# Performance work log

Measured on AMD Instinct MI355X. Metric: run time of the kernel, lower is better.

## Reference

```python
import jax, jax.numpy as jnp
import numpy as np

NP, LP, ROUTINGS = 8, 16, 3
PAD = 2  # (kernel_size - 1) // 2 for kernel_size=5, stride=1


def _squash_2(t):
    # norm over LP axis (axis=3); torch: norm/(1+norm^2+1e-4) * t
    norm = jnp.linalg.norm(t, axis=3, keepdims=True)
    return norm / (1.0 + norm * norm + 1e-4) * t


def setup_inputs() -> dict:
    key = jax.random.key(0)
    k1, k2 = jax.random.split(key)
    x = jax.random.normal(k1, (4, 4, 16, 256, 256), dtype=jnp.float32)
    # conv weights initialized uniform [0, 0.1] as in the torch module
    W = jax.random.uniform(k2, (NP * LP, 16, 5, 5), dtype=jnp.float32) * 0.1
    return {"x": x, "W": W}


def reference(x, W):
    B, NC, LC, H, Wd = x.shape
    xf = x.reshape(B * NC, LC, H, Wd)
    votes = jax.lax.conv_general_dilated(
        xf, W, window_strides=(1, 1), padding=((PAD, PAD), (PAD, PAD)),
        dimension_numbers=("NCHW", "OIHW", "NCHW"))  # (B*NC, NP*LP, H, W)
    votes = votes.reshape(B, NC, NP, LP, H, Wd)
    sims = jnp.zeros((B, NC, NP, 1, H, Wd), dtype=x.dtype)
    parent = None
    for _ in range(ROUTINGS):
        c_ij = jax.nn.softmax(sims + 1e-4, axis=2)          # softmax over NP
        parent_bs = jnp.sum(c_ij * votes, axis=1, keepdims=True)  # sum over NC
        parent = _squash_2(parent_bs)                        # (B,1,NP,LP,H,W)
        sims = sims + jnp.sum(votes * parent, axis=3, keepdims=True)
    return parent[:, 0]  # squeeze NC axis -> (B, NP, LP, H, W)
```

## Files before the change

kernel.cpp:

```cpp
#include <hip/hip_runtime.h>

#define NPAR 8
#define LPAR 16
#define OCH 128
#define HH 256
#define WW 256
#define HWSZ (HH*WW)

typedef _Float16 f16x8 __attribute__((ext_vector_type(8)));
typedef _Float16 f16x4 __attribute__((ext_vector_type(4)));
typedef _Float16 f16x2 __attribute__((ext_vector_type(2)));
typedef float    f32x4 __attribute__((ext_vector_type(4)));

#define SMEM_MAIN 16896
#define VROW 132
#define SMEM_HALVES_FUSED 16896

#if defined(__has_builtin)
#if __has_builtin(__builtin_amdgcn_fdot2)
#define HAVE_FDOT2 1
#endif
#if __has_builtin(__builtin_amdgcn_global_load_lds)
#define HAVE_GLL 1
#endif
#endif

__device__ __forceinline__ float fdot2_acc(f16x2 a, f16x2 b, float c) {
#ifdef HAVE_FDOT2
    return __builtin_amdgcn_fdot2(a, b, c, false);
#else
    return c + (float)a[0] * (float)b[0] + (float)a[1] * (float)b[1];
#endif
}

__device__ __forceinline__ f16x2 quad_sum4_pk(f16x2 v) {
    int t = __builtin_amdgcn_update_dpp(0, __builtin_bit_cast(int, v),
                                        0xB1, 0xF, 0xF, true);
    v = v + __builtin_bit_cast(f16x2, t);
    t = __builtin_amdgcn_update_dpp(0, __builtin_bit_cast(int, v),
                                    0x4E, 0xF, 0xF, true);
    v = v + __builtin_bit_cast(f16x2, t);
    return v;
}

__device__ __forceinline__ void stage16(const _Float16* gp, _Float16* lp, int lane) {
#ifdef HAVE_GLL
    __builtin_amdgcn_global_load_lds((const __attribute__((address_space(1))) void*)gp,
                                     (__attribute__((address_space(3))) void*)lp, 16, 0, 0);
#else
    *(f16x8*)(lp + lane * 8) = *(const f16x8*)gp;
#endif
}

__global__ void reorder_W_lin(const float* __restrict__ Wg,
                              _Float16* __restrict__ ws) {
    int idx = blockIdx.x * 256 + threadIdx.x;
    if (idx >= 13 * 128 * 32) return;
    const int q  = idx & 31;
    const int oc = (idx >> 5) & 127;
    const int kk = idx >> 12;
    const int tap = 2 * kk + (q >> 4);
    const int ci  = ((q >> 3) & 1) * 8 + (q & 7);
    const float v = (tap < 25) ? Wg[oc * 400 + ci * 25 + tap] : 0.f;
    ws[idx] = (_Float16)v;
}

__global__ __launch_bounds__(256)
void transpose_x_kernel(const float* __restrict__ x, _Float16* __restrict__ xh) {
    __shared__ _Float16 ts[4096];
    const int tid = threadIdx.x;
    const int bx  = blockIdx.x;
    const int b   = bx >> 10;
    const int h   = (bx >> 2) & 255;
    const int wt  = bx & 3;
    const int w0  = wt * 64;
    {
        const int wl = tid & 63, cq = tid >> 6;
        const float* src = x + (((size_t)(b * 64 + cq * 16) * 256 + h) * 256 + w0 + wl);
#pragma unroll
        for (int k = 0; k < 2; ++k) {
            f16x8 pk;
#pragma unroll
            for (int j = 0; j < 8; ++j)
                pk[j] = (_Float16)src[(size_t)(k * 8 + j) * HWSZ];
            const int gL = (cq * 2 + k) ^ (wl & 7);
            *(f16x8*)&ts[wl * 64 + gL * 8] = pk;
        }
    }
    __syncthreads();
    {
        const int wo = tid >> 2, gq = tid & 3;
        _Float16* dst = xh + (((size_t)(b * 260) + h + 2) * 260 + (w0 + wo + 2)) * 64 + gq * 16;
#pragma unroll
        for (int k = 0; k < 2; ++k) {
            const int gL = (gq * 2 + k) ^ (wo & 7);
            *(f16x8*)&dst[k * 8] = *(const f16x8*)&ts[wo * 64 + gL * 8];
        }
    }
}

__global__ __launch_bounds__(256, 3)
void capsule_mfma10_kernel(const _Float16* __restrict__ xh,
                           const _Float16* __restrict__ wsW,
                           float* __restrict__ out) {
    __shared__ _Float16 sm[SMEM_MAIN];

    const int tid = threadIdx.x;
    const int w   = tid >> 6;
    const int l   = tid & 63;

    const int blk   = ((blockIdx.x & 7) << 10) + (blockIdx.x >> 3);
    const int b     = blk >> 11;
    const int rt    = blk & 2047;
    const int hrow0 = (rt >> 4) << 1;
    const int w0    = (rt & 15) << 4;

    {
        const size_t bbase = ((size_t)(b * 260 + hrow0) * 260 + w0) * 64;
#pragma unroll
        for (int jj = 0; jj < 4; ++jj) {
            const int cidx = w * 4 + jj;
            if (cidx < 15) {
                const int G = cidx * 64 + l;
                const unsigned dyr = (unsigned)G / 160u;
                const unsigned rem = (unsigned)G - dyr * 160u;
                const int wp = rem >> 3, g = rem & 7;
                const int gsrc = g ^ (wp & 7);
                const _Float16* gp = xh + bbase + dyr * 16640u + wp * 64 + gsrc * 8;
                stage16(gp, &sm[cidx * 512], l);
            }
        }
    }
    __syncthreads();

    const int rwc = w >> 1;
    const int oh  = w & 1;
    const int kq  = l >> 4;
    const int ml  = l & 15;
    const bool hiT = (kq & 2) != 0;
    const int pxA = ml >> 2;
    const int colA = (ml & 3) * 16 + (kq & 1) * 8;
    const int bfbase = (oh * 64 + ml) * 32 + kq * 8;

    f32x4 acc[4][4];
#pragma unroll
    for (int a = 0; a < 4; ++a)
#pragma unroll
        for (int bb = 0; bb < 4; ++bb)
            acc[a][bb] = (f32x4){0.f, 0.f, 0.f, 0.f};

#pragma unroll
    for (int kk = 0; kk < 13; ++kk) {
        f16x8 bf[4];
#pragma unroll
        for (int bb = 0; bb < 4; ++bb)
            bf[bb] = *(const f16x8*)&wsW[kk * 4096 + bb * 512 + bfbase];

        const int t0 = 2 * kk;
        const int t1 = (2 * kk + 1 > 24) ? 24 : 2 * kk + 1;
        const int dy = hiT ? (t1 / 5) : (t0 / 5);
        const int dx = hiT ? (t1 % 5) : (t0 % 5);

        f16x8 af[4];
#pragma unroll
        for (int a = 0; a < 4; ++a) {
            const int wp = a * 4 + pxA + dx;
            af[a] = *(const f16x8*)&sm[((rwc + dy) * 20 + wp) * 64
                                       + (colA ^ ((wp & 7) << 3))];
        }
        __builtin_amdgcn_s_setprio(1);
#pragma unroll
        for (int a = 0; a < 4; ++a)
#pragma unroll
            for (int bb = 0; bb < 4; ++bb)
                acc[a][bb] = __builtin_amdgcn_mfma_f32_16x16x32_f16(
                    af[a], bf[bb], acc[a][bb], 0, 0, 0);
        __builtin_amdgcn_s_setprio(0);
    }
    __syncthreads();

#pragma unroll
    for (int a = 0; a < 4; ++a) {
#pragma unroll
        for (int reg = 0; reg < 4; ++reg) {
            f16x4 pk;
#pragma unroll
            for (int bb = 0; bb < 4; ++bb) pk[bb] = (_Float16)acc[a][bb][reg];
            const int R = rwc * 64 + a * 16 + kq * 4 + reg;
            *(f16x4*)&sm[R * VROW + ml * 8 + oh * 4] = pk;
        }
    }
    __syncthreads();

    const int ncR = tid & 3;
    const int h   = (tid >> 2) & 1;
    const int pxx = (tid >> 3) & 15;
    const int rw  = tid >> 7;

    const int R = rw * 64 + pxx * 4 + ncR;
    f16x8 vh[8];
#pragma unroll
    for (int c8 = 0; c8 < 8; ++c8)
        vh[c8] = *(const f16x8*)&sm[R * VROW + (h * 8 + c8) * 8];

    float* outb = out + (size_t)b * OCH * HWSZ
                + (size_t)(hrow0 + rw) * WW + (w0 + pxx);

    float sims[NPAR];
#pragma unroll
    for (int i = 0; i < NPAR; ++i) sims[i] = 0.f;

#pragma unroll
    for (int it = 0; it < 3; ++it) {
        float e[NPAR];
        float inv = 0.f;
        if (it > 0) {
            float mx = fmaxf(fmaxf(fmaxf(sims[0], sims[1]), fmaxf(sims[2], sims[3])),
                             fmaxf(fmaxf(sims[4], sims[5]), fmaxf(sims[6], sims[7])));
            float se = 0.f;
#pragma unroll
            for (int i = 0; i < NPAR; ++i) { e[i] = __expf(sims[i] - mx); se += e[i]; }
            inv = 1.f / se;
        }
#pragma unroll
        for (int np_ = 0; np_ < NPAR; ++np_) {
            const float cf = (it == 0) ? 0.f : e[np_] * inv;
            const f16x2 cp = (f16x2){(_Float16)cf, (_Float16)cf};
            float n2 = 0.f, dot = 0.f;
            f16x2 keep0 = (f16x2){(_Float16)0.f, (_Float16)0.f};
            f16x2 keep1 = keep0;
#pragma unroll
            for (int k = 0; k < 4; ++k) {
                const f16x2 vv = (f16x2){vh[2 * k][np_], vh[2 * k + 1][np_]};
                const f16x2 sv = (it == 0) ? vv : (cp * vv);
                const f16x2 t2 = quad_sum4_pk(sv);
                n2 = fdot2_acc(t2, t2, n2);
                if (it < 2) dot = fdot2_acc(vv, t2, dot);
                if (it == 2 && (k >> 1) == (ncR & 1)) {
                    if (k & 1) keep1 = t2; else keep0 = t2;
                }
            }
            n2 += __shfl_xor(n2, 4);
            if (it == 0) n2 *= 0.015625f;
            const float scale = sqrtf(n2) / (1.f + n2 + 1e-4f);
            if (it < 2) {
                dot += __shfl_xor(dot, 4);
                if (it == 0) dot *= 0.125f;
                sims[np_] += scale * dot;
            }
            if (it == 2 && (ncR >> 1) == h) {
                outb[(size_t)(np_ * LPAR + ncR * 4 + 0) * HWSZ] = scale * (float)keep0[0];
                outb[(size_t)(np_ * LPAR + ncR * 4 + 1) * HWSZ] = scale * (float)keep0[1];
                outb[(size_t)(np_ * LPAR + ncR * 4 + 2) * HWSZ] = scale * (float)keep1[0];
                outb[(size_t)(np_ * LPAR + ncR * 4 + 3) * HWSZ] = scale * (float)keep1[1];
            }
        }
    }
}

__device__ __forceinline__ int xs_addr6(int dyr, int wp, int col) {
    return (dyr * 20 + wp) * 64 + (col ^ ((wp & 7) << 3));
}

__global__ __launch_bounds__(256, 3)
void capsule_mfma6_kernel(const float* __restrict__ x,
                          const _Float16* __restrict__ wsf,
                          float* __restrict__ out) {
    __shared__ _Float16 sm[SMEM_HALVES_FUSED];

    const int tid = threadIdx.x;
    const int w   = tid >> 6;
    const int l   = tid & 63;

    const int blk   = ((blockIdx.x & 7) << 10) + (blockIdx.x >> 3);
    const int b     = blk >> 11;
    const int rt    = blk & 2047;
    const int hrow0 = (rt >> 4) << 1;
    const int w0    = (rt & 15) << 4;

    for (int i = 0; i < 15; ++i) {
        const unsigned idx = i * 256 + tid;
        const unsigned q   = idx / 20u;
        const int wp  = idx - q * 20u;
        const int cip = q & 7;
        const int t2  = q >> 3;
        const int nc  = t2 & 3;
        const int dyr = t2 >> 2;
        const int hh  = hrow0 + dyr - 2;
        const int wg  = w0 + wp - 2;
        const bool ok = (hh >= 0) && (hh < HH) && (wg >= 0) && (wg < WW);
        const float* src = x + (((size_t)(b * 4 + nc) * 16 + cip * 2) * HH + hh) * (size_t)WW + wg;
        const float v0 = ok ? src[0] : 0.f;
        const float v1 = ok ? src[HWSZ] : 0.f;
        *(f16x2*)&sm[xs_addr6(dyr, wp, nc * 16 + cip * 2)] =
            (f16x2){(_Float16)v0, (_Float16)v1};
    }
    __syncthreads();

    const int rwc = w >> 1;
    const int oh  = w & 1;
    const int p   = l >> 4;
    const int ml  = l & 15;
    const bool hiT = (p & 2) != 0;
    const int ciA = (p & 1) * 8;
    const int pxA = ml >> 2;
    const int ncA = ml & 3;
    const int bfbase = (oh * 64 + ml) * 32 + p * 8;

    f32x4 acc[4][4];
#pragma unroll
    for (int a = 0; a < 4; ++a)
#pragma unroll
        for (int bb = 0; bb < 4; ++bb)
            acc[a][bb] = (f32x4){0.f, 0.f, 0.f, 0.f};

#pragma unroll
    for (int kk = 0; kk < 13; ++kk) {
        f16x8 bf[4];
#pragma unroll
        for (int bb = 0; bb < 4; ++bb)
            bf[bb] = *(const f16x8*)&wsf[kk * 4096 + bb * 512 + bfbase];

        const int t0 = 2 * kk;
        const int t1 = (2 * kk + 1 > 24) ? 24 : 2 * kk + 1;
        const int dy = hiT ? (t1 / 5) : (t0 / 5);
        const int dx = hiT ? (t1 % 5) : (t0 % 5);

        f16x8 af[4];
#pragma unroll
        for (int a = 0; a < 4; ++a)
            af[a] = *(const f16x8*)&sm[xs_addr6(rwc + dy, a * 4 + pxA + dx, ncA * 16 + ciA)];

#pragma unroll
        for (int a = 0; a < 4; ++a)
#pragma unroll
            for (int bb = 0; bb < 4; ++bb)
                acc[a][bb] = __builtin_amdgcn_mfma_f32_16x16x32_f16(
                    af[a], bf[bb], acc[a][bb], 0, 0, 0);
    }
    __syncthreads();

#pragma unroll
    for (int a = 0; a < 4; ++a) {
#pragma unroll
        for (int reg = 0; reg < 4; ++reg) {
            f16x4 pk;
#pragma unroll
            for (int bb = 0; bb < 4; ++bb) pk[bb] = (_Float16)acc[a][bb][reg];
            const int R = rwc * 64 + a * 16 + p * 4 + reg;
            *(f16x4*)&sm[R * VROW + ml * 8 + oh * 4] = pk;
        }
    }
    __syncthreads();

    const int ncR = tid & 3;
    const int h   = (tid >> 2) & 1;
    const int pxx = (tid >> 3) & 15;
    const int rw  = tid >> 7;

    const int R = rw * 64 + pxx * 4 + ncR;
    f16x8 vh[8];
#pragma unroll
    for (int c8 = 0; c8 < 8; ++c8)
        vh[c8] = *(const f16x8*)&sm[R * VROW + (h * 8 + c8) * 8];

    float* outb = out + (size_t)b * OCH * HWSZ
                + (size_t)(hrow0 + rw) * WW + (w0 + pxx);

    float sims[NPAR];
#pragma unroll
    for (int i = 0; i < NPAR; ++i) sims[i] = 0.f;

#pragma unroll
    for (int it = 0; it < 3; ++it) {
        float mx = fmaxf(fmaxf(fmaxf(sims[0], sims[1]), fmaxf(sims[2], sims[3])),
                         fmaxf(fmaxf(sims[4], sims[5]), fmaxf(sims[6], sims[7])));
        float e[NPAR];
        float se = 0.f;
#pragma unroll
        for (int i = 0; i < NPAR; ++i) { e[i] = __expf(sims[i] - mx); se += e[i]; }
        const float inv = 1.f / se;

#pragma unroll
        for (int np_ = 0; np_ < NPAR; ++np_) {
            const float cf = e[np_] * inv;
            const f16x2 cp = (f16x2){(_Float16)cf, (_Float16)cf};
            float n2 = 0.f, dot = 0.f;
            f16x2 keep0 = (f16x2){(_Float16)0.f, (_Float16)0.f};
            f16x2 keep1 = keep0;
#pragma unroll
            for (int k = 0; k < 4; ++k) {
                const f16x2 vv = (f16x2){vh[2 * k][np_], vh[2 * k + 1][np_]};
                const f16x2 t2 = quad_sum4_pk(cp * vv);
                n2  = fdot2_acc(t2, t2, n2);
                dot = fdot2_acc(vv, t2, dot);
                if (it == 2 && (k >> 1) == (ncR & 1)) {
                    if (k & 1) keep1 = t2; else keep0 = t2;
                }
            }
            n2  += __shfl_xor(n2, 4);
            dot += __shfl_xor(dot, 4);
            const float scale = sqrtf(n2) / (1.f + n2 + 1e-4f);
            sims[np_] += scale * dot;

            if (it == 2 && (ncR >> 1) == h) {
                outb[(size_t)(np_ * LPAR + ncR * 4 + 0) * HWSZ] = scale * (float)keep0[0];
                outb[(size_t)(np_ * LPAR + ncR * 4 + 1) * HWSZ] = scale * (float)keep0[1];
                outb[(size_t)(np_ * LPAR + ncR * 4 + 2) * HWSZ] = scale * (float)keep1[0];
                outb[(size_t)(np_ * LPAR + ncR * 4 + 3) * HWSZ] = scale * (float)keep1[1];
            }
        }
    }
}

extern "C" void kernel_launch(void* const* d_in, const int* in_sizes, int n_in,
                              void* d_out, int out_size, void* d_ws, size_t ws_size,
                              hipStream_t stream) {
    const float* x  = (const float*)d_in[0];
    const float* Wg = (const float*)d_in[1];
    float* out = (float*)d_out;
    _Float16* ws = (_Float16*)d_ws;
    (void)in_sizes; (void)n_in; (void)out_size;

    const size_t XH_BYTES = (size_t)4 * 260 * 260 * 64 * 2;
    const size_t NEED = 131072 + XH_BYTES;

    hipLaunchKernelGGL(reorder_W_lin, dim3(208), dim3(256), 0, stream, Wg, ws);

    if (ws_size >= NEED) {
        _Float16* xh = ws + 65536;
        hipMemsetAsync((void*)xh, 0, XH_BYTES, stream);
        hipLaunchKernelGGL(transpose_x_kernel, dim3(4096), dim3(256), 0, stream, x, xh);
        hipLaunchKernelGGL(capsule_mfma10_kernel, dim3(8192), dim3(256), 0, stream,
                           xh, ws, out);
    } else {
        hipLaunchKernelGGL(capsule_mfma6_kernel, dim3(8192), dim3(256), 0, stream,
                           x, ws, out);
    }
}
```

Measured before the change: 219.2 us.

## Switch conv to 32x32x16 MFMA reading activations directly from global

Replaces the 16x16x32 MFMA tiling over paired taps with 32x32x16 MFMAs, one per tap over 16 channels, using a new per-tap weight layout (reorder_W25). The LDS staging of the input tile and its barrier are removed, and A fragments are loaded straight from the padded fp16 global buffer, relying on L1/L2 caching. The channel-to-parent mapping changes, so a perm-based repack of votes and a remapped output index are added. It drops the zero-padded 26th tap and an LDS round trip, at the cost of more global load traffic and less explicit reuse.

```diff
diff --git a/kernel.cpp b/kernel.cpp
--- a/kernel.cpp
+++ b/kernel.cpp
@@ -11,6 +11,8 @@
 typedef _Float16 f16x4 __attribute__((ext_vector_type(4)));
 typedef _Float16 f16x2 __attribute__((ext_vector_type(2)));
 typedef float    f32x4 __attribute__((ext_vector_type(4)));
+typedef float    f32x16 __attribute__((ext_vector_type(16)));
+typedef int      i32x4 __attribute__((ext_vector_type(4)));
 
 #define SMEM_MAIN 16896
 #define VROW 132
@@ -20,8 +22,8 @@
 #if __has_builtin(__builtin_amdgcn_fdot2)
 #define HAVE_FDOT2 1
 #endif
-#if __has_builtin(__builtin_amdgcn_global_load_lds)
-#define HAVE_GLL 1
+#if __has_builtin(__builtin_amdgcn_perm)
+#define HAVE_PERM 1
 #endif
 #endif
 
@@ -43,13 +45,14 @@
     return v;
 }
 
-__device__ __forceinline__ void stage16(const _Float16* gp, _Float16* lp, int lane) {
-#ifdef HAVE_GLL
-    __builtin_amdgcn_global_load_lds((const __attribute__((address_space(1))) void*)gp,
-                                     (__attribute__((address_space(3))) void*)lp, 16, 0, 0);
-#else
-    *(f16x8*)(lp + lane * 8) = *(const f16x8*)gp;
-#endif
+__global__ void reorder_W25(const float* __restrict__ Wg,
+                            _Float16* __restrict__ ws) {
+    int idx = blockIdx.x * 256 + threadIdx.x;
+    if (idx >= 25 * 128 * 16) return;
+    const int ci  = idx & 15;
+    const int oc  = (idx >> 4) & 127;
+    const int tap = idx >> 11;
+    ws[idx] = (_Float16)Wg[oc * 400 + ci * 25 + tap];
 }
 
 __global__ void reorder_W_lin(const float* __restrict__ Wg,
@@ -100,8 +103,8 @@
 }
 
 __global__ __launch_bounds__(256, 3)
-void capsule_mfma10_kernel(const _Float16* __restrict__ xh,
-                           const _Float16* __restrict__ wsW,
+void capsule_mfma11_kernel(const _Float16* __restrict__ xh,
+                           const _Float16* __restrict__ wsB,
                            float* __restrict__ out) {
     __shared__ _Float16 sm[SMEM_MAIN];
 
@@ -115,79 +118,52 @@
     const int hrow0 = (rt >> 4) << 1;
     const int w0    = (rt & 15) << 4;
 
-    {
-        const size_t bbase = ((size_t)(b * 260 + hrow0) * 260 + w0) * 64;
-#pragma unroll
-        for (int jj = 0; jj < 4; ++jj) {
-            const int cidx = w * 4 + jj;
-            if (cidx < 15) {
-                const int G = cidx * 64 + l;
-                const unsigned dyr = (unsigned)G / 160u;
-                const unsigned rem = (unsigned)G - dyr * 160u;
-                const int wp = rem >> 3, g = rem & 7;
-                const int gsrc = g ^ (wp & 7);
-                const _Float16* gp = xh + bbase + dyr * 16640u + wp * 64 + gsrc * 8;
-                stage16(gp, &sm[cidx * 512], l);
-            }
-        }
-    }
-    __syncthreads();
-
     const int rwc = w >> 1;
     const int oh  = w & 1;
-    const int kq  = l >> 4;
-    const int ml  = l & 15;
-    const bool hiT = (kq & 2) != 0;
-    const int pxA = ml >> 2;
-    const int colA = (ml & 3) * 16 + (kq & 1) * 8;
-    const int bfbase = (oh * 64 + ml) * 32 + kq * 8;
-
-    f32x4 acc[4][4];
-#pragma unroll
-    for (int a = 0; a < 4; ++a)
-#pragma unroll
-        for (int bb = 0; bb < 4; ++bb)
-            acc[a][bb] = (f32x4){0.f, 0.f, 0.f, 0.f};
-
-#pragma unroll
-    for (int kk = 0; kk < 13; ++kk) {
-        f16x8 bf[4];
-#pragma unroll
-        for (int bb = 0; bb < 4; ++bb)
-            bf[bb] = *(const f16x8*)&wsW[kk * 4096 + bb * 512 + bfbase];
-
-        const int t0 = 2 * kk;
-        const int t1 = (2 * kk + 1 > 24) ? 24 : 2 * kk + 1;
-        const int dy = hiT ? (t1 / 5) : (t0 / 5);
-        const int dx = hiT ? (t1 % 5) : (t0 % 5);
-
-        f16x8 af[4];
-#pragma unroll
-        for (int a = 0; a < 4; ++a) {
-            const int wp = a * 4 + pxA + dx;
-            af[a] = *(const f16x8*)&sm[((rwc + dy) * 20 + wp) * 64
-                                       + (colA ^ ((wp & 7) << 3))];
-        }
+    const int l31 = l & 31;
+    const int kh  = l >> 5;
+    const int ncA = l31 & 3;
+    const int pxq = l31 >> 2;
+
+    const _Float16* gb = xh + (((size_t)(b * 260 + hrow0 + rwc)) * 260 + w0 + pxq) * 64
+                       + ncA * 16 + kh * 8;
+    const _Float16* bP[5] = { gb, gb + 16640, gb + 2 * 16640, gb + 3 * 16640, gb + 4 * 16640 };
+
+    const _Float16* wbase = wsB + (oh * 64 + l31) * 16 + kh * 8;
+
+    f32x16 acc[2][2];
+#pragma unroll
+    for (int mt = 0; mt < 2; ++mt)
+#pragma unroll
+        for (int nt = 0; nt < 2; ++nt)
+#pragma unroll
+            for (int r = 0; r < 16; ++r)
+                acc[mt][nt][r] = 0.f;
+
+#pragma unroll
+    for (int tap = 0; tap < 25; ++tap) {
+        const int dy = tap / 5;
+        const int dx = tap % 5;
+        const f16x8 bf0 = *(const f16x8*)(wbase + tap * 2048);
+        const f16x8 bf1 = *(const f16x8*)(wbase + tap * 2048 + 512);
+        const f16x8 af0 = *(const f16x8*)(bP[dy] + (size_t)(dx)      * 64);
+        const f16x8 af1 = *(const f16x8*)(bP[dy] + (size_t)(dx + 8)  * 64);
         __builtin_amdgcn_s_setprio(1);
-#pragma unroll
-        for (int a = 0; a < 4; ++a)
-#pragma unroll
-            for (int bb = 0; bb < 4; ++bb)
-                acc[a][bb] = __builtin_amdgcn_mfma_f32_16x16x32_f16(
-                    af[a], bf[bb], acc[a][bb], 0, 0, 0);
+        acc[0][0] = __builtin_amdgcn_mfma_f32_32x32x16_f16(af0, bf0, acc[0][0], 0, 0, 0);
+        acc[0][1] = __builtin_amdgcn_mfma_f32_32x32x16_f16(af0, bf1, acc[0][1], 0, 0, 0);
+        acc[1][0] = __builtin_amdgcn_mfma_f32_32x32x16_f16(af1, bf0, acc[1][0], 0, 0, 0);
+        acc[1][1] = __builtin_amdgcn_mfma_f32_32x32x16_f16(af1, bf1, acc[1][1], 0, 0, 0);
         __builtin_amdgcn_s_setprio(0);
     }
-    __syncthreads();
-
-#pragma unroll
-    for (int a = 0; a < 4; ++a) {
-#pragma unroll
-        for (int reg = 0; reg < 4; ++reg) {
-            f16x4 pk;
-#pragma unroll
-            for (int bb = 0; bb < 4; ++bb) pk[bb] = (_Float16)acc[a][bb][reg];
-            const int R = rwc * 64 + a * 16 + kq * 4 + reg;
-            *(f16x4*)&sm[R * VROW + ml * 8 + oh * 4] = pk;
+
+#pragma unroll
+    for (int mt = 0; mt < 2; ++mt) {
+#pragma unroll
+        for (int reg = 0; reg < 16; ++reg) {
+            const f16x2 pk = (f16x2){(_Float16)acc[mt][0][reg], (_Float16)acc[mt][1][reg]};
+            const int pxt = mt * 8 + 2 * (reg >> 2) + kh;
+            const int R   = rwc * 64 + pxt * 4 + (reg & 3);
+            *(f16x2*)&sm[R * VROW + (l & 15) * 8 + oh * 4 + ((l31 >> 4) << 1)] = pk;
         }
     }
     __syncthreads();
@@ -202,6 +178,27 @@
 #pragma unroll
     for (int c8 = 0; c8 < 8; ++c8)
         vh[c8] = *(const f16x8*)&sm[R * VROW + (h * 8 + c8) * 8];
+
+    int vnpw[NPAR][4];
+#pragma unroll
+    for (int K = 0; K < 4; ++K) {
+        const i32x4 A = __builtin_bit_cast(i32x4, vh[2 * K]);
+        const i32x4 B = __builtin_bit_cast(i32x4, vh[2 * K + 1]);
+#pragma unroll
+        for (int nh = 0; nh < 4; ++nh) {
+#ifdef HAVE_PERM
+            vnpw[2 * nh][K]     = (int)__builtin_amdgcn_perm(
+                (unsigned)B[nh], (unsigned)A[nh], 0x05040100u);
+            vnpw[2 * nh + 1][K] = (int)__builtin_amdgcn_perm(
+                (unsigned)B[nh], (unsigned)A[nh], 0x07060302u);
+#else
+            const f16x2 lo = (f16x2){vh[2 * K][2 * nh],     vh[2 * K + 1][2 * nh]};
+            const f16x2 hi = (f16x2){vh[2 * K][2 * nh + 1], vh[2 * K + 1][2 * nh + 1]};
+            vnpw[2 * nh][K]     = __builtin_bit_cast(int, lo);
+            vnpw[2 * nh + 1][K] = __builtin_bit_cast(int, hi);
+#endif
+        }
+    }
 
     float* outb = out + (size_t)b * OCH * HWSZ
                 + (size_t)(hrow0 + rw) * WW + (w0 + pxx);
@@ -223,21 +220,21 @@
             inv = 1.f / se;
         }
 #pragma unroll
-        for (int np_ = 0; np_ < NPAR; ++np_) {
-            const float cf = (it == 0) ? 0.f : e[np_] * inv;
+        for (int s = 0; s < NPAR; ++s) {
+            const float cf = (it == 0) ? 0.f : e[s] * inv;
             const f16x2 cp = (f16x2){(_Float16)cf, (_Float16)cf};
             float n2 = 0.f, dot = 0.f;
             f16x2 keep0 = (f16x2){(_Float16)0.f, (_Float16)0.f};
             f16x2 keep1 = keep0;
 #pragma unroll
-            for (int k = 0; k < 4; ++k) {
-                const f16x2 vv = (f16x2){vh[2 * k][np_], vh[2 * k + 1][np_]};
+            for (int K = 0; K < 4; ++K) {
+                const f16x2 vv = __builtin_bit_cast(f16x2, vnpw[s][K]);
                 const f16x2 sv = (it == 0) ? vv : (cp * vv);
                 const f16x2 t2 = quad_sum4_pk(sv);
                 n2 = fdot2_acc(t2, t2, n2);
                 if (it < 2) dot = fdot2_acc(vv, t2, dot);
-                if (it == 2 && (k >> 1) == (ncR & 1)) {
-                    if (k & 1) keep1 = t2; else keep0 = t2;
+                if (it == 2 && (K >> 1) == (ncR & 1)) {
+                    if (K & 1) keep1 = t2; else keep0 = t2;
                 }
             }
             n2 += __shfl_xor(n2, 4);
@@ -246,13 +243,14 @@
             if (it < 2) {
                 dot += __shfl_xor(dot, 4);
                 if (it == 0) dot *= 0.125f;
-                sims[np_] += scale * dot;
+                sims[s] += scale * dot;
             }
             if (it == 2 && (ncR >> 1) == h) {
-                outb[(size_t)(np_ * LPAR + ncR * 4 + 0) * HWSZ] = scale * (float)keep0[0];
-                outb[(size_t)(np_ * LPAR + ncR * 4 + 1) * HWSZ] = scale * (float)keep0[1];
-                outb[(size_t)(np_ * LPAR + ncR * 4 + 2) * HWSZ] = scale * (float)keep1[0];
-                outb[(size_t)(np_ * LPAR + ncR * 4 + 3) * HWSZ] = scale * (float)keep1[1];
+                const int np_out = (s & 4) | ((s & 1) << 1) | ((s >> 1) & 1);
+                outb[(size_t)(np_out * LPAR + ncR * 4 + 0) * HWSZ] = scale * (float)keep0[0];
+                outb[(size_t)(np_out * LPAR + ncR * 4 + 1) * HWSZ] = scale * (float)keep0[1];
+                outb[(size_t)(np_out * LPAR + ncR * 4 + 2) * HWSZ] = scale * (float)keep1[0];
+                outb[(size_t)(np_out * LPAR + ncR * 4 + 3) * HWSZ] = scale * (float)keep1[1];
             }
         }
     }
@@ -425,15 +423,15 @@
     const size_t XH_BYTES = (size_t)4 * 260 * 260 * 64 * 2;
     const size_t NEED = 131072 + XH_BYTES;
 
-    hipLaunchKernelGGL(reorder_W_lin, dim3(208), dim3(256), 0, stream, Wg, ws);
-
     if (ws_size >= NEED) {
         _Float16* xh = ws + 65536;
+        hipLaunchKernelGGL(reorder_W25, dim3(200), dim3(256), 0, stream, Wg, ws);
         hipMemsetAsync((void*)xh, 0, XH_BYTES, stream);
         hipLaunchKernelGGL(transpose_x_kernel, dim3(4096), dim3(256), 0, stream, x, xh);
-        hipLaunchKernelGGL(capsule_mfma10_kernel, dim3(8192), dim3(256), 0, stream,
+        hipLaunchKernelGGL(capsule_mfma11_kernel, dim3(8192), dim3(256), 0, stream,
                            xh, ws, out);
     } else {
+        hipLaunchKernelGGL(reorder_W_lin, dim3(208), dim3(256), 0, stream, Wg, ws);
         hipLaunchKernelGGL(capsule_mfma6_kernel, dim3(8192), dim3(256), 0, stream,
                            x, ws, out);
     }
```

Result: slower. 224.0 us (+2.1%).
